# Performance work log

Hardware: AMD Instinct MI355X
Metric: run time of the kernel (lower is better)

Reference implementation:

```python
import jax, jax.numpy as jnp
import numpy as np

UNITS = 32      # 12 inter + 19 command + 1 motor
SENSORY = 32    # dense_2 output dim
MOTOR = 1
ODE_UNFOLDS = 6
EPS = 1e-8


def _build_wiring():
    # kerasncp NCP wiring: motor ids [0,1), command [1,20), inter [20,32)
    rng = np.random.RandomState(42)
    inter = np.arange(20, 32)
    command = np.arange(1, 20)
    motor = np.arange(0, 1)
    adj = np.zeros((UNITS, UNITS), np.float32)
    sens = np.zeros((SENSORY, UNITS), np.float32)
    for s in range(SENSORY):                      # sensory_fanout=6 onto inter neurons
        for d in rng.choice(inter, 6, replace=False):
            sens[s, d] = rng.choice([-1.0, 1.0])
    for i in inter:                               # inter_fanout=4 onto command neurons
        for d in rng.choice(command, 4, replace=False):
            adj[i, d] = rng.choice([-1.0, 1.0])
    for _ in range(6):                            # 6 recurrent command synapses
        adj[rng.choice(command), rng.choice(command)] = rng.choice([-1.0, 1.0])
    for m in motor:                               # motor_fanin=4 from command neurons
        for srcn in rng.choice(command, 4, replace=False):
            adj[srcn, m] = rng.choice([-1.0, 1.0])
    return adj, sens


def setup_inputs() -> dict:
    key = jax.random.key(0)
    ks = jax.random.split(key, 12)
    B, T = 256, 1024
    adj, sens = _build_wiring()
    u = lambda k, sh, lo, hi: jax.random.uniform(k, sh, jnp.float32, lo, hi)
    return {
        "x": jax.random.normal(ks[0], (B, T, 2), jnp.float32),
        "d1_w": jax.random.normal(ks[1], (2, 128), jnp.float32) * (1.0 / np.sqrt(2.0)),
        "d1_b": jnp.zeros((128,), jnp.float32),
        "d2_w": jax.random.normal(ks[2], (128, SENSORY), jnp.float32) * (1.0 / np.sqrt(128.0)),
        "d2_b": jnp.zeros((SENSORY,), jnp.float32),
        "input_w": jnp.ones((SENSORY,), jnp.float32),
        "input_b": jnp.zeros((SENSORY,), jnp.float32),
        "output_w": jnp.ones((MOTOR,), jnp.float32),
        "output_b": jnp.zeros((MOTOR,), jnp.float32),
        "gleak": u(ks[3], (UNITS,), 0.001, 1.0),
        "vleak": u(ks[4], (UNITS,), -0.2, 0.2),
        "cm": u(ks[5], (UNITS,), 0.4, 0.6),
        "w_syn": u(ks[6], (UNITS, UNITS), 0.001, 1.0),
        "mu": u(ks[7], (UNITS, UNITS), 0.3, 0.8),
        "sigma": u(ks[8], (UNITS, UNITS), 3.0, 8.0),
        "erev": jnp.asarray(adj),
        "sensory_w": u(ks[9], (SENSORY, UNITS), 0.001, 1.0),
        "sensory_mu": u(ks[10], (SENSORY, UNITS), 0.3, 0.8),
        "sensory_sigma": u(ks[11], (SENSORY, UNITS), 3.0, 8.0),
        "sensory_erev": jnp.asarray(sens),
        "sparsity_mask": jnp.asarray(np.abs(adj), jnp.int32),
        "sensory_mask": jnp.asarray(np.abs(sens), jnp.int32),
    }


def reference(x, d1_w, d1_b, d2_w, d2_b, input_w, input_b, output_w, output_b,
              gleak, vleak, cm, w_syn, mu, sigma, erev,
              sensory_w, sensory_mu, sensory_sigma, sensory_erev,
              sparsity_mask, sensory_mask):
    # Dense stack (per timestep)
    h = jax.nn.relu(x @ d1_w + d1_b)          # [B,T,128]
    h = h @ d2_w + d2_b                        # [B,T,32] sensory inputs
    spm = sparsity_mask.astype(h.dtype)
    ssm = sensory_mask.astype(h.dtype)

    def gate(v, m, s):                         # v [B,pre] -> [B,pre,post]
        return jax.nn.sigmoid(s * (v[..., None] - m))

    cm_t = cm * ODE_UNFOLDS                    # cm / (elapsed_time / ode_unfolds), elapsed_time=1

    def step(v, xt):
        inp = xt * input_w + input_b           # LTC input mapping (affine)
        sa = sensory_w * gate(inp, sensory_mu, sensory_sigma) * ssm   # [B,32,32]
        wnum_s = jnp.sum(sa * sensory_erev, axis=1)                   # [B,32]
        wden_s = jnp.sum(sa, axis=1)

        def unfold(vp, _):
            wa = w_syn * gate(vp, mu, sigma) * spm                    # [B,32,32]
            wnum = jnp.sum(wa * erev, axis=1) + wnum_s
            wden = jnp.sum(wa, axis=1) + wden_s
            vp = (cm_t * vp + gleak * vleak + wnum) / (cm_t + gleak + wden + EPS)
            return vp, None

        v, _ = jax.lax.scan(unfold, v, None, length=ODE_UNFOLDS)
        return v, None

    v0 = jnp.zeros((h.shape[0], UNITS), h.dtype)
    vT, _ = jax.lax.scan(step, v0, jnp.swapaxes(h, 0, 1))  # scan over T
    # output mapping: motor neurons are the first MOTOR states
    return vT[:, :MOTOR] * output_w + output_b             # [B,1]
```

## Files before the change

kernel.cpp:

```cpp
#include <hip/hip_runtime.h>
#include <math.h>

#define NB 256
#define NT 1024
#define NUNF 6
#define TBS 128
#define CHK 8
#define NTJMAX 12
#define L2E 1.44269504088896340736f
#define PI_F 3.14159265358979324f

typedef const float* fp;

extern "C" __device__ float __ocml_exp2_f32(float);
__device__ __forceinline__ float frcp(float x) { return __builtin_amdgcn_rcpf(x); }
__device__ __forceinline__ float ex2(float x) { return __ocml_exp2_f32(x); }
__device__ __forceinline__ float sgm(float a, float b, float v) { return frcp(1.f + ex2(fmaf(a, v, b))); }

struct Tables {
    int ngroups, npos, nchunks, ntraj;
    int grp_start[21];
    int ord[20];
    int pos[20];
    int aff[20];
    int need_traj[20];
    int traj_slot[20];
    int ch_ps[20], ch_pe[20], ch_gs[20], ch_ge[20];
    int ncp[20], nip[20], ngp[20];
    float cmt[20], cn0[20], cd0[20];
    float icmt[12];
    int   cp_pre[20][8];
    float cp_a[20][8], cp_b[20][8], cp_w[20][8], cp_e[20][8];
    int   ip_i[20][12];
    float ip_a[20][12], ip_b[20][12], ip_w[20][12], ip_e[20][12];
    int   gp_pre[20][6];
    float gp_a[20][6], gp_b[20][6], gp_w[20][6], gp_e[20][6];
};

struct DenseTab {
    int cnt[12];
    float in0[12], id0[12];
    int   pre[12][32];
    float a[12][32], b[12][32], w[12][32], e[12][32];
    int homog, maxcnt;
};

#define WS_DTAB   16384
#define WS_BND    24576
#define WS_BMASK  25600
#define WS_MG     32768
#define WS_VST    98304
#define WS_SENSI  131072

__global__ void build_tables(fp wsyn, fp mu, fp sigma, fp erev, const int* spm,
                             fp sw, fp smu, fp ssg, fp serev, const int* smask,
                             fp cm, fp gleak, fp vleak, fp d1b, Tables* T, DenseTab* D) {
    __shared__ int   spmL[1024], smkL[1024];
    __shared__ float wL[1024], muL[1024], sgL[1024], evL[1024];
    __shared__ float swL[1024], smuL[1024], ssgL[1024], sevL[1024];
    __shared__ float cmL[32], glL[32], vlL[32];
    __shared__ int premaskL[20], ancL[20], rootL[20], depUL[20], keyL[20], posL[20], ordL[20];
    __shared__ int ngpL[20], ntjL[20], slotU[20];
    __shared__ int neededS;
    __shared__ float habs[64];
    __shared__ int cntS[12];
    int tid = threadIdx.x;
    for (int k = tid; k < 1024; k += 64) {
        spmL[k] = spm[k]; wL[k] = wsyn[k]; muL[k] = mu[k]; sgL[k] = sigma[k]; evL[k] = erev[k];
        smkL[k] = smask[k]; swL[k] = sw[k]; smuL[k] = smu[k]; ssgL[k] = ssg[k]; sevL[k] = serev[k];
    }
    if (tid < 32) { cmL[tid] = cm[tid]; glL[tid] = gleak[tid]; vlL[tid] = vleak[tid]; }
    habs[tid] = fmaxf(fabsf(d1b[tid]), fabsf(d1b[tid + 64]));
    __syncthreads();
    if (tid < 20) {
        int pm = 0;
        for (int i = 0; i < 20; ++i) if (spmL[i * 32 + tid]) pm |= 1 << i;
        premaskL[tid] = pm;
        ancL[tid] = pm;
    }
    __syncthreads();
    for (int it = 0; it < 20; ++it) {
        int a = 0;
        if (tid < 20) {
            a = ancL[tid];
            int pm = premaskL[tid];
            for (int i = 0; i < 20; ++i) if ((pm >> i) & 1) a |= ancL[i];
        }
        __syncthreads();
        if (tid < 20) ancL[tid] = a;
        __syncthreads();
    }
    if (tid == 0) neededS = ancL[0] | 1;
    __syncthreads();
    int needed = neededS;
    if (tid < 20) {
        int r = tid;
        if ((needed >> tid) & 1) {
            int aj = ancL[tid];
            for (int i = 0; i < 20; ++i)
                if (i < r && ((needed >> i) & 1) && ((aj >> i) & 1) && ((ancL[i] >> tid) & 1)) r = i;
        }
        rootL[tid] = r;
        depUL[tid] = 0;
    }
    __syncthreads();
    for (int it = 0; it < 21; ++it) {
        int d = 0;
        if (tid < 20 && ((needed >> tid) & 1)) {
            int pm = premaskL[tid], myr = rootL[tid];
            for (int i = 0; i < 20; ++i)
                if (((pm >> i) & 1) && rootL[i] != myr) d = max(d, depUL[i] + 1);
        }
        __syncthreads();
        if (tid < 20 && d > depUL[tid]) depUL[tid] = d;
        __syncthreads();
    }
    if (tid < 20) {
        int key = 0x7FFFFFFF;
        if ((needed >> tid) & 1) {
            int myr = rootL[tid], dg = 0;
            for (int i = 0; i < 20; ++i)
                if (((needed >> i) & 1) && rootL[i] == myr) dg = max(dg, depUL[i]);
            key = dg * 32 + myr;
        }
        keyL[tid] = key;
    }
    __syncthreads();
    if (tid < 20) {
        int mykey = keyL[tid];
        int p = 0;
        for (int k = 0; k < 20; ++k)
            if (keyL[k] < mykey || (keyL[k] == mykey && k < tid)) ++p;
        posL[tid] = p;
        if (p < 20) ordL[p] = tid;
    }
    __syncthreads();
    if (tid < 20) {
        int nt = 0;
        if ((needed >> tid) & 1)
            for (int j = 0; j < 20; ++j)
                if (j != tid && ((needed >> j) & 1) && spmL[tid * 32 + j]) { nt = 1; break; }
        ntjL[tid] = nt;
    }
    __syncthreads();
    if (tid == 0) {
        int s = 0;
        for (int p = 0; p < 20; ++p) { int u = ordL[p]; slotU[u] = s; s += ntjL[u]; }
        T->ntraj = s;
    }
    __syncthreads();
    if (tid < 20) {
        int j = tid, cc = 0, ci = 0, cg = 0;
        T->cmt[j] = cmL[j] * (float)NUNF;
        T->cn0[j] = glL[j] * vlL[j];
        T->cd0[j] = cmL[j] * (float)NUNF + glL[j] + 1e-8f;
        if ((needed >> j) & 1) {
            int myr = rootL[j];
            int mystart = posL[myr];
            for (int i = 0; i < 32; ++i) {
                int p = i * 32 + j;
                if (!spmL[p]) continue;
                float sg = sgL[p];
                float a = -sg * L2E, b = sg * muL[p] * L2E;
                float w = wL[p], e = w * evL[p];
                if (i >= 20) {
                    T->ip_i[j][ci] = i - 20;
                    T->ip_a[j][ci] = a; T->ip_b[j][ci] = b; T->ip_w[j][ci] = w; T->ip_e[j][ci] = e;
                    ++ci;
                } else if (rootL[i] == myr) {
                    T->gp_pre[j][cg] = posL[i] - mystart;
                    T->gp_a[j][cg] = a; T->gp_b[j][cg] = b; T->gp_w[j][cg] = w; T->gp_e[j][cg] = e;
                    ++cg;
                } else {
                    T->cp_pre[j][cc] = slotU[i];
                    T->cp_a[j][cc] = a; T->cp_b[j][cc] = b; T->cp_w[j][cc] = w; T->cp_e[j][cc] = e;
                    ++cc;
                }
            }
        }
        T->ncp[j] = cc; T->nip[j] = ci; T->ngp[j] = cg;
        ngpL[j] = cg;
    }
    if (tid < 12) {
        T->icmt[tid] = cmL[20 + tid] * (float)NUNF;
        int unit = 20 + tid, cnt = 0;
        for (int s = 0; s < 32; ++s) {
            int p = s * 32 + unit;
            if (!smkL[p]) continue;
            float sg = ssgL[p];
            D->pre[tid][cnt] = s;
            D->a[tid][cnt] = -sg * L2E;
            D->b[tid][cnt] = sg * smuL[p] * L2E;
            D->w[tid][cnt] = swL[p];
            D->e[tid][cnt] = swL[p] * sevL[p];
            ++cnt;
        }
        for (int c = cnt; c < 32; ++c) {
            D->pre[tid][c] = 0; D->a[tid][c] = 0.f; D->b[tid][c] = 0.f;
            D->w[tid][c] = 0.f; D->e[tid][c] = 0.f;
        }
        D->cnt[tid] = cnt;
        cntS[tid] = cnt;
        D->in0[tid] = glL[unit] * vlL[unit];
        D->id0[tid] = cmL[unit] * (float)NUNF + glL[unit] + 1e-8f;
    }
    __syncthreads();
    if (tid == 0) {
        int npos = __popc(needed & 0xFFFFF);
        T->npos = npos;
        int ng = 0, prevkey = -1;
        for (int p = 0; p < npos; ++p) {
            int u = ordL[p];
            if (keyL[u] != prevkey) { T->grp_start[ng] = p; ++ng; prevkey = keyL[u]; }
        }
        T->ngroups = ng;
        for (int g = ng; g <= 20; ++g) T->grp_start[g] = npos;
        for (int p = 0; p < 20; ++p) T->ord[p] = (p < npos) ? ordL[p] : 0;
        for (int j = 0; j < 20; ++j) T->pos[j] = posL[j];
        for (int g = 0; g < ng; ++g) {
            int gs = T->grp_start[g], ge = T->grp_start[g + 1], gsz = ge - gs;
            for (int p = gs; p < ge; ++p)
                T->aff[p] = (gsz == 1 && ngpL[ordL[p]] == 0) ? 1 : 0;
        }
        for (int p = npos; p < 20; ++p) T->aff[p] = 0;
        for (int p = 0; p < 20; ++p) {
            int u = ordL[p];
            T->need_traj[p] = ntjL[u];
            T->traj_slot[p] = slotU[u];
        }
        int nchunks = 0, g = 0;
        while (g < ng) {
            int lvl = keyL[ordL[T->grp_start[g]]] / 32;
            int ge = g;
            while (ge < ng && keyL[ordL[T->grp_start[ge]]] / 32 == lvl) ++ge;
            int cs = g;
            while (cs < ge) {
                int ce = cs, acc = 0;
                while (ce < ge) {
                    int gsz = T->grp_start[ce + 1] - T->grp_start[ce];
                    if (acc + gsz > CHK && ce > cs) break;
                    acc += gsz; ++ce;
                    if (acc >= CHK) break;
                }
                T->ch_gs[nchunks] = cs; T->ch_ge[nchunks] = ce;
                T->ch_ps[nchunks] = T->grp_start[cs]; T->ch_pe[nchunks] = T->grp_start[ce];
                ++nchunks;
                cs = ce;
            }
            g = ge;
        }
        T->nchunks = nchunks;
        float hm = 0.f;
        for (int k = 0; k < 64; ++k) hm = fmaxf(hm, habs[k]);
        D->homog = (hm == 0.f) ? 1 : 0;
        int mc = 0;
        for (int k = 0; k < 12; ++k) mc = max(mc, cntS[k]);
        D->maxcnt = mc;
    }
}

__global__ void sector_prep(fp d1w, float* bnd, int* bmask) {
    __shared__ float ang[256];
    __shared__ float uS[128], vS[128];
    int tid = threadIdx.x;
    if (tid < 128) { uS[tid] = d1w[tid]; vS[tid] = d1w[128 + tid]; }
    __syncthreads();
    {
        int k = tid & 127;
        float al = atan2f(vS[k], uS[k]);
        float bb = (tid < 128) ? al + 1.57079632679489662f : al - 1.57079632679489662f;
        if (bb > PI_F) bb -= 2.f * PI_F;
        if (bb <= -PI_F) bb += 2.f * PI_F;
        ang[tid] = bb;
    }
    __syncthreads();
    for (int k = 2; k <= 256; k <<= 1) {
        for (int j = k >> 1; j > 0; j >>= 1) {
            int ixj = tid ^ j;
            if (ixj > tid) {
                float a0 = ang[tid], a1 = ang[ixj];
                bool up = ((tid & k) == 0);
                if ((a0 > a1) == up) { ang[tid] = a1; ang[ixj] = a0; }
            }
            __syncthreads();
        }
    }
    bnd[tid] = ang[tid];
    float lo = ang[tid];
    float hi = (tid < 255) ? ang[tid + 1] : ang[0] + 2.f * PI_F;
    float tm = 0.5f * (lo + hi);
    float ct = cosf(tm), st = sinf(tm);
    for (int w = 0; w < 4; ++w) {
        int m = 0;
        for (int kk = 0; kk < 32; ++kk) {
            int k = w * 32 + kk;
            if (fmaf(uS[k], ct, vS[k] * st) > 0.f) m |= 1 << kk;
        }
        bmask[tid * 4 + w] = m;
    }
}

__global__ void sector_M(fp d1w, fp d2w, fp iw, const int* bmask, float2* Mg) {
    int s = blockIdx.x, j = threadIdx.x;
    if (j >= 32) return;
    float acc0 = 0.f, acc1 = 0.f;
#pragma unroll
    for (int w = 0; w < 4; ++w) {
        int mm = bmask[s * 4 + w];
        for (int kk = 0; kk < 32; ++kk) {
            if ((mm >> kk) & 1) {
                int k = w * 32 + kk;
                float w2 = d2w[k * 32 + j];
                acc0 = fmaf(d1w[k], w2, acc0);
                acc1 = fmaf(d1w[128 + k], w2, acc1);
            }
        }
    }
    float iwj = iw[j];
    Mg[s * 32 + j] = make_float2(acc0 * iwj, acc1 * iwj);
}

__global__ __launch_bounds__(256) void dense_homog(
    fp x, fp d2b, fp iw, fp ib,
    const DenseTab* __restrict__ Dg, const float2* __restrict__ Mg, const float* __restrict__ bndg,
    float2* sensI, int t0, int CT) {
    if (Dg->homog == 0) return;
    __shared__ float bndL[256];
    __shared__ float4 tabT[416];
    __shared__ int   preT[416];
    __shared__ float ibuf[4][2112];
    __shared__ float b2q[32], iwq[32], ibq[32];
    __shared__ float in0L[12], id0L[12];
    int tid = threadIdx.x;
    for (int idx = tid; idx < 384; idx += 256) {
        int d = idx >> 5, e = idx & 31;
        int sl = e * 13 + d;
        tabT[sl] = make_float4(Dg->a[d][e], Dg->b[d][e], Dg->w[d][e], Dg->e[d][e]);
        preT[sl] = Dg->pre[d][e];
    }
    if (tid < 12) { in0L[tid] = Dg->in0[tid]; id0L[tid] = Dg->id0[tid]; }
    if (tid < 32) { b2q[tid] = d2b[tid]; iwq[tid] = iw[tid]; ibq[tid] = ib[tid]; }
    if (tid < 256) bndL[tid] = bndg[tid];
    __syncthreads();
    int wid = tid >> 6, lane = tid & 63;
    const float2* x2 = (const float2*)x;
    int gw = blockIdx.x * 4 + wid;
    int nw = gridDim.x * 4;
    float* ibf = ibuf[wid];
    int jj = lane & 31, h = lane >> 5;
    float cj = fmaf(b2q[jj], iwq[jj], ibq[jj]);
    int cntmax = Dg->maxcnt;
    int pass_total = (NB * CT) >> 6;
    for (int pass = gw; pass < pass_total; pass += nw) {
        int cg0 = pass * 64;
        int cg = cg0 + lane;
        int lt = cg >> 8, bb_ = cg & 255;
        float2 xv = x2[bb_ * NT + (t0 + lt)];
        float th = atan2f(xv.y, xv.x);
        int sec;
        if (th < bndL[0]) sec = 255;
        else {
            int lo = 0, hi = 255;
#pragma unroll
            for (int it7 = 0; it7 < 8; ++it7) {
                int mid = (lo + hi + 1) >> 1;
                if (bndL[mid] <= th) lo = mid; else hi = mid - 1;
            }
            sec = lo;
        }
        float x0r = xv.x, x1r = xv.y;
#pragma unroll 4
        for (int r = 0; r < 32; ++r) {
            int item = 2 * r + h;
            int s_it = __shfl(sec, item);
            float xi0 = __shfl(x0r, item);
            float xi1 = __shfl(x1r, item);
            float2 m = Mg[s_it * 32 + jj];
            ibf[item * 33 + jj] = fmaf(xi0, m.x, fmaf(xi1, m.y, cj));
        }
        __builtin_amdgcn_wave_barrier();
#pragma unroll
        for (int rb = 0; rb < 12; ++rb) {
            int task = rb * 64 + lane;
            int item = task / 12;
            int dd = task - item * 12;
            float wn = in0L[dd], wd = id0L[dd];
            for (int e = 0; e < cntmax; ++e) {
                int sl = e * 13 + dd;
                float4 tb = tabT[sl];
                float pv = ibf[item * 33 + preT[sl]];
                float gq = frcp(1.f + ex2(fmaf(tb.x, pv, tb.y)));
                wn = fmaf(tb.w, gq, wn);
                wd = fmaf(tb.z, gq, wd);
            }
            int cg2 = cg0 + item;
            int lt2 = cg2 >> 8, b2_ = cg2 & 255;
            sensI[(size_t)(b2_ * CT + lt2) * 12 + dd] = make_float2(wn, wd);
        }
        __builtin_amdgcn_wave_barrier();
    }
}

__global__ __launch_bounds__(256) void dense_general(
    fp x, fp d1w, fp d1b, fp d2w, fp d2b, fp iw, fp ib,
    const DenseTab* __restrict__ Dg, float2* sensI, int t0, int CT) {
    if (Dg->homog != 0) return;
    __shared__ float W2s[4096];
    __shared__ float W1s[256], b1s[128];
    __shared__ float b2q[32], iwq[32], ibq[32];
    __shared__ float4 tabT[416];
    __shared__ int   preT[416];
    __shared__ int   cntL[12];
    __shared__ float in0L[12], id0L[12];
    __shared__ float hbuf[4][128][20];
    __shared__ float ibuf[4][16][33];
    int tid = threadIdx.x;
    for (int idx = tid; idx < 384; idx += 256) {
        int d = idx >> 5, e = idx & 31;
        int sl = e * 13 + d;
        tabT[sl] = make_float4(Dg->a[d][e], Dg->b[d][e], Dg->w[d][e], Dg->e[d][e]);
        preT[sl] = Dg->pre[d][e];
    }
    if (tid < 12) { cntL[tid] = Dg->cnt[tid]; in0L[tid] = Dg->in0[tid]; id0L[tid] = Dg->id0[tid]; }
    for (int p = tid; p < 4096; p += 256) W2s[p] = d2w[p];
    if (tid < 256) W1s[tid] = d1w[tid];
    if (tid < 128) b1s[tid] = d1b[tid];
    if (tid < 32) { b2q[tid] = d2b[tid]; iwq[tid] = iw[tid]; ibq[tid] = ib[tid]; }
    __syncthreads();
    int wid = tid >> 6, lane = tid & 63;
    float* hb = (float*)hbuf[wid];
    float* ibf = (float*)ibuf[wid];
    const float2* x2 = (const float2*)x;
    int gw = blockIdx.x * 4 + wid;
    int nw = gridDim.x * 4;
    int pass_total = (NB * CT) >> 4;
    int itd1 = lane >> 2, kq = lane & 3;
    int j = lane & 31, half = lane >> 5;
    for (int pass = gw; pass < pass_total; pass += nw) {
        int cg0 = pass * 16;
        {
            int cg = cg0 + itd1;
            int lt = cg >> 8, b = cg & 255;
            float2 xv = x2[b * NT + (t0 + lt)];
#pragma unroll 8
            for (int i = 0; i < 32; ++i) {
                int k = kq + 4 * i;
                float hk = fmaf(xv.y, W1s[128 + k], fmaf(xv.x, W1s[k], b1s[k]));
                hb[k * 20 + itd1] = hk > 0.f ? hk : 0.f;
            }
        }
        __builtin_amdgcn_wave_barrier();
        {
            float a0=0,a1=0,a2=0,a3=0,a4=0,a5=0,a6=0,a7=0;
#pragma unroll 4
            for (int k = 0; k < 128; ++k) {
                float w2 = W2s[k * 32 + j];
                float4 ha = *(const float4*)&hb[k * 20 + half * 8];
                float4 hbv = *(const float4*)&hb[k * 20 + half * 8 + 4];
                a0 = fmaf(ha.x, w2, a0); a1 = fmaf(ha.y, w2, a1);
                a2 = fmaf(ha.z, w2, a2); a3 = fmaf(ha.w, w2, a3);
                a4 = fmaf(hbv.x, w2, a4); a5 = fmaf(hbv.y, w2, a5);
                a6 = fmaf(hbv.z, w2, a6); a7 = fmaf(hbv.w, w2, a7);
            }
            float bb = b2q[j], iww = iwq[j], ibb = ibq[j];
            ibf[(half*8+0)*33+j] = fmaf(a0+bb, iww, ibb);
            ibf[(half*8+1)*33+j] = fmaf(a1+bb, iww, ibb);
            ibf[(half*8+2)*33+j] = fmaf(a2+bb, iww, ibb);
            ibf[(half*8+3)*33+j] = fmaf(a3+bb, iww, ibb);
            ibf[(half*8+4)*33+j] = fmaf(a4+bb, iww, ibb);
            ibf[(half*8+5)*33+j] = fmaf(a5+bb, iww, ibb);
            ibf[(half*8+6)*33+j] = fmaf(a6+bb, iww, ibb);
            ibf[(half*8+7)*33+j] = fmaf(a7+bb, iww, ibb);
        }
        __builtin_amdgcn_wave_barrier();
#pragma unroll
        for (int r = 0; r < 3; ++r) {
            int task = r * 64 + lane;
            int it = task / 12;
            int d = task - it * 12;
            int cnt = cntL[d];
            float wn = in0L[d], wd = id0L[d];
            for (int e = 0; e < cnt; ++e) {
                int sl = e * 13 + d;
                float4 tb = tabT[sl];
                float gq = frcp(1.f + ex2(fmaf(tb.x, ibf[it * 33 + preT[sl]], tb.y)));
                wn = fmaf(tb.w, gq, wn);
                wd = fmaf(tb.z, gq, wd);
            }
            int cg = cg0 + it;
            int lt = cg >> 8, b = cg & 255;
            sensI[(size_t)(b * CT + lt) * 12 + d] = make_float2(wn, wd);
        }
        __builtin_amdgcn_wave_barrier();
    }
}

__global__ __launch_bounds__(512) void solve(const float2* __restrict__ sensI,
                                             const Tables* __restrict__ Tg,
                                             fp ow, fp ob, float* vstate,
                                             int t0, int CT, float* out) {
    __shared__ Tables TL;
    __shared__ float2 iAB[TBS * 12];
    __shared__ float viter[TBS * 13];
    __shared__ float vtraj[NTJMAX * TBS * 7];
    __shared__ float2 pnpd[CHK * TBS * 7];
    __shared__ float2 comp[CHK * TBS];
    __shared__ float vstart[CHK * TBS];
    __shared__ float gstate[20], istate[12];
    int tid = threadIdx.x;
    int b = blockIdx.x;
    {
        const int nw = (int)(sizeof(Tables) / 4);
        const int* src = (const int*)Tg;
        int* dst = (int*)&TL;
        for (int k = tid; k < nw; k += 512) dst[k] = src[k];
    }
    __syncthreads();
    if (tid < 20 && tid < TL.npos)
        gstate[tid] = (t0 == 0) ? 0.f : vstate[b * 32 + TL.ord[tid]];
    if (tid < 12)
        istate[tid] = (t0 == 0) ? 0.f : vstate[b * 32 + 20 + tid];
    __syncthreads();
    int ntiles = CT / TBS;
    bool lastChunk = (t0 + CT == NT);
    for (int tile = 0; tile < ntiles; ++tile) {
        int tbase = tile * TBS;
        for (int w = tid; w < TBS * 16; w += 512) {
            int tt = w >> 4, ii = w & 15;
            if (ii < 12) {
                float2 s = sensI[(size_t)(b * CT + tbase + tt) * 12 + ii];
                float r = frcp(s.y);
                iAB[tt * 12 + ii] = make_float2(TL.icmt[ii] * r, s.x * r);
            }
        }
        __syncthreads();
        if (tid < 12) {
            float v = istate[tid];
#pragma unroll 4
            for (int tt = 0; tt < TBS; ++tt) {
                float2 ab = iAB[tt * 12 + tid];
                float A = ab.x, B = ab.y;
                float A2 = A * A, A4 = A2 * A2;
                float A6 = A4 * A2;
                float B6 = B * (1.f + A) * (1.f + A2 + A4);
                viter[tt * 13 + tid] = v;
                v = fmaf(A6, v, B6);
            }
            istate[tid] = v;
        }
        __syncthreads();
        int nchunks = TL.nchunks;
        for (int c = 0; c < nchunks; ++c) {
            int ps = TL.ch_ps[c], pe = TL.ch_pe[c];
            int gs0 = TL.ch_gs[c], ge0 = TL.ch_ge[c];
            int npc = pe - ps;
            for (int w = tid; w < npc * TBS; w += 512) {
                int m = w >> 7, tt = w & (TBS - 1);
                int posi = ps + m;
                int unit = TL.ord[posi];
                float pn[6], pd[6];
#pragma unroll
                for (int u = 0; u < 6; ++u) { pn[u] = TL.cn0[unit]; pd[u] = TL.cd0[unit]; }
                int ncp = TL.ncp[unit];
                for (int e = 0; e < ncp; ++e) {
                    int sl = TL.cp_pre[unit][e];
                    float a = TL.cp_a[unit][e], bb = TL.cp_b[unit][e];
                    float w_ = TL.cp_w[unit][e], ev = TL.cp_e[unit][e];
#pragma unroll
                    for (int u = 0; u < 6; ++u) {
                        float gq = sgm(a, bb, vtraj[(sl * TBS + tt) * 7 + u]);
                        pn[u] = fmaf(ev, gq, pn[u]);
                        pd[u] = fmaf(w_, gq, pd[u]);
                    }
                }
                int nip = TL.nip[unit];
                for (int e = 0; e < nip; ++e) {
                    int ii = TL.ip_i[unit][e];
                    float2 ab = iAB[tt * 12 + ii];
                    float vi = viter[tt * 13 + ii];
                    float a = TL.ip_a[unit][e], bb = TL.ip_b[unit][e];
                    float w_ = TL.ip_w[unit][e], ev = TL.ip_e[unit][e];
#pragma unroll
                    for (int u = 0; u < 6; ++u) {
                        float gq = sgm(a, bb, vi);
                        pn[u] = fmaf(ev, gq, pn[u]);
                        pd[u] = fmaf(w_, gq, pd[u]);
                        vi = fmaf(ab.x, vi, ab.y);
                    }
                }
                if (TL.aff[posi]) {
                    float cmt = TL.cmt[unit];
                    float Ac = 1.f, Bc = 0.f;
#pragma unroll
                    for (int u = 0; u < 6; ++u) {
                        float r = frcp(pd[u]);
                        float Au = cmt * r, Bu = pn[u] * r;
                        pnpd[(m * TBS + tt) * 7 + u] = make_float2(Au, Bu);
                        Bc = fmaf(Au, Bc, Bu);
                        Ac *= Au;
                    }
                    comp[m * TBS + tt] = make_float2(Ac, Bc);
                } else {
#pragma unroll
                    for (int u = 0; u < 6; ++u)
                        pnpd[(m * TBS + tt) * 7 + u] = make_float2(pn[u], pd[u]);
                }
            }
            __syncthreads();
            if (tid < ge0 - gs0) {
                int g = gs0 + tid;
                int gs = TL.grp_start[g], ge = TL.grp_start[g + 1], gsz = ge - gs;
                int m0 = gs - ps;
                if (gsz == 1) {
                    int unit = TL.ord[gs];
                    float v = gstate[gs];
                    if (TL.aff[gs]) {
#pragma unroll 4
                        for (int tt = 0; tt < TBS; ++tt) {
                            vstart[m0 * TBS + tt] = v;
                            float2 cc = comp[m0 * TBS + tt];
                            v = fmaf(cc.x, v, cc.y);
                        }
                    } else {
                        float ga = TL.gp_a[unit][0], gb = TL.gp_b[unit][0];
                        float gw = TL.gp_w[unit][0], gev = TL.gp_e[unit][0];
                        float cmt = TL.cmt[unit];
                        int ntj = TL.need_traj[gs];
                        int sl = TL.traj_slot[gs];
                        for (int tt = 0; tt < TBS; ++tt) {
#pragma unroll
                            for (int u = 0; u < 6; ++u) {
                                if (ntj) vtraj[(sl * TBS + tt) * 7 + u] = v;
                                float2 pp2 = pnpd[(m0 * TBS + tt) * 7 + u];
                                float E = ex2(fmaf(ga, v, gb));
                                float P = fmaf(cmt, v, pp2.x);
                                float N = fmaf(P, E, P + gev);
                                float Dd = fmaf(pp2.y, E, pp2.y + gw);
                                v = N * frcp(Dd);
                            }
                        }
                    }
                    gstate[gs] = v;
                } else {
                    float sv[CHK], nv[CHK];
#pragma unroll
                    for (int mm = 0; mm < CHK; ++mm) if (mm < gsz) sv[mm] = gstate[gs + mm];
                    for (int tt = 0; tt < TBS; ++tt) {
#pragma unroll
                        for (int u = 0; u < 6; ++u) {
#pragma unroll
                            for (int mm = 0; mm < CHK; ++mm)
                                if (mm < gsz && TL.need_traj[gs + mm])
                                    vtraj[(TL.traj_slot[gs + mm] * TBS + tt) * 7 + u] = sv[mm];
#pragma unroll
                            for (int mm = 0; mm < CHK; ++mm) {
                                if (mm < gsz) {
                                    int unit = TL.ord[gs + mm];
                                    float2 pp2 = pnpd[((m0 + mm) * TBS + tt) * 7 + u];
                                    float wn = pp2.x, wd = pp2.y;
                                    int ngpu = TL.ngp[unit];
#pragma unroll
                                    for (int e = 0; e < 6; ++e) {
                                        if (e < ngpu) {
                                            float vp = sv[TL.gp_pre[unit][e]];
                                            float gq = sgm(TL.gp_a[unit][e], TL.gp_b[unit][e], vp);
                                            wn = fmaf(TL.gp_e[unit][e], gq, wn);
                                            wd = fmaf(TL.gp_w[unit][e], gq, wd);
                                        }
                                    }
                                    nv[mm] = fmaf(TL.cmt[unit], sv[mm], wn) * frcp(wd);
                                }
                            }
#pragma unroll
                            for (int mm = 0; mm < CHK; ++mm) if (mm < gsz) sv[mm] = nv[mm];
                        }
                    }
#pragma unroll
                    for (int mm = 0; mm < CHK; ++mm) if (mm < gsz) gstate[gs + mm] = sv[mm];
                }
            }
            __syncthreads();
            for (int w = tid; w < npc * TBS; w += 512) {
                int m = w >> 7, tt = w & (TBS - 1);
                int posi = ps + m;
                if (TL.aff[posi] && TL.need_traj[posi]) {
                    int sl = TL.traj_slot[posi];
                    float v = vstart[m * TBS + tt];
#pragma unroll
                    for (int u = 0; u < 6; ++u) {
                        vtraj[(sl * TBS + tt) * 7 + u] = v;
                        float2 ab = pnpd[(m * TBS + tt) * 7 + u];
                        v = fmaf(ab.x, v, ab.y);
                    }
                }
            }
            __syncthreads();
        }
    }
    if (tid < 20 && tid < TL.npos) vstate[b * 32 + TL.ord[tid]] = gstate[tid];
    if (tid < 12) vstate[b * 32 + 20 + tid] = istate[tid];
    if (lastChunk) {
        __syncthreads();
        if (tid == 0) out[b] = fmaf(gstate[TL.pos[0]], ow[0], ob[0]);
    }
}

extern "C" void kernel_launch(void* const* d_in, const int* in_sizes, int n_in,
                              void* d_out, int out_size, void* d_ws, size_t ws_size,
                              hipStream_t stream) {
    fp x     = (fp)d_in[0];
    fp d1w   = (fp)d_in[1];
    fp d1b   = (fp)d_in[2];
    fp d2w   = (fp)d_in[3];
    fp d2b   = (fp)d_in[4];
    fp iw    = (fp)d_in[5];
    fp ib    = (fp)d_in[6];
    fp ow    = (fp)d_in[7];
    fp ob    = (fp)d_in[8];
    fp gleak = (fp)d_in[9];
    fp vleak = (fp)d_in[10];
    fp cm    = (fp)d_in[11];
    fp wsyn  = (fp)d_in[12];
    fp mu    = (fp)d_in[13];
    fp sigma = (fp)d_in[14];
    fp erev  = (fp)d_in[15];
    fp sw    = (fp)d_in[16];
    fp smu   = (fp)d_in[17];
    fp ssg   = (fp)d_in[18];
    fp serev = (fp)d_in[19];
    const int* spm   = (const int*)d_in[20];
    const int* smask = (const int*)d_in[21];

    char* wsb = (char*)d_ws;
    Tables*   T = (Tables*)wsb;
    DenseTab* D = (DenseTab*)(wsb + WS_DTAB);
    float*   bnd = (float*)(wsb + WS_BND);
    int*   bmask = (int*)(wsb + WS_BMASK);
    float2*   Mg = (float2*)(wsb + WS_MG);
    float* vstate = (float*)(wsb + WS_VST);
    float2* sensI = (float2*)(wsb + WS_SENSI);

    size_t per_t = (size_t)NB * 12 * sizeof(float2);
    int CT = TBS;
    if (ws_size > WS_SENSI) {
        size_t m = (ws_size - WS_SENSI) / per_t;
        int ct = TBS;
        while (ct < NT && (size_t)(ct * 2) <= m) ct *= 2;
        CT = ct;
    }

    build_tables<<<1, 64, 0, stream>>>(wsyn, mu, sigma, erev, spm,
                                       sw, smu, ssg, serev, smask,
                                       cm, gleak, vleak, d1b, T, D);
    sector_prep<<<1, 256, 0, stream>>>(d1w, bnd, bmask);
    sector_M<<<256, 64, 0, stream>>>(d1w, d2w, iw, bmask, Mg);

    int nch = NT / CT;
    for (int c = 0; c < nch; ++c) {
        int t0 = c * CT;
        dense_homog<<<768, 256, 0, stream>>>(x, d2b, iw, ib, D, Mg, bnd, sensI, t0, CT);
        dense_general<<<512, 256, 0, stream>>>(x, d1w, d1b, d2w, d2b, iw, ib, D, sensI, t0, CT);
        solve<<<NB, 512, 0, stream>>>(sensI, T, ow, ob, vstate, t0, CT, (float*)d_out);
    }
}
```

Before: 276.0 us.

## Fuse homogeneous sensory dense stage into the solve kernel per tile

Removes the separate dense_homog kernel and computes the sensory synapse sums inside solve for each 128-step tile, writing iAB directly from shared memory instead of round-tripping through the global sensI buffer. This drops one launch per chunk and the global write/read of the sensory intermediates. In exchange, the per-batch solve block now does the atan2, sector search and gating work itself, serially before each tile's recurrence, which adds shared-memory pressure and lengthens the solve kernel's critical path.

```diff
diff --git a/kernel.cpp b/kernel.cpp
--- a/kernel.cpp
+++ b/kernel.cpp
@@ -320,87 +320,6 @@
     Mg[s * 32 + j] = make_float2(acc0 * iwj, acc1 * iwj);
 }
 
-__global__ __launch_bounds__(256) void dense_homog(
-    fp x, fp d2b, fp iw, fp ib,
-    const DenseTab* __restrict__ Dg, const float2* __restrict__ Mg, const float* __restrict__ bndg,
-    float2* sensI, int t0, int CT) {
-    if (Dg->homog == 0) return;
-    __shared__ float bndL[256];
-    __shared__ float4 tabT[416];
-    __shared__ int   preT[416];
-    __shared__ float ibuf[4][2112];
-    __shared__ float b2q[32], iwq[32], ibq[32];
-    __shared__ float in0L[12], id0L[12];
-    int tid = threadIdx.x;
-    for (int idx = tid; idx < 384; idx += 256) {
-        int d = idx >> 5, e = idx & 31;
-        int sl = e * 13 + d;
-        tabT[sl] = make_float4(Dg->a[d][e], Dg->b[d][e], Dg->w[d][e], Dg->e[d][e]);
-        preT[sl] = Dg->pre[d][e];
-    }
-    if (tid < 12) { in0L[tid] = Dg->in0[tid]; id0L[tid] = Dg->id0[tid]; }
-    if (tid < 32) { b2q[tid] = d2b[tid]; iwq[tid] = iw[tid]; ibq[tid] = ib[tid]; }
-    if (tid < 256) bndL[tid] = bndg[tid];
-    __syncthreads();
-    int wid = tid >> 6, lane = tid & 63;
-    const float2* x2 = (const float2*)x;
-    int gw = blockIdx.x * 4 + wid;
-    int nw = gridDim.x * 4;
-    float* ibf = ibuf[wid];
-    int jj = lane & 31, h = lane >> 5;
-    float cj = fmaf(b2q[jj], iwq[jj], ibq[jj]);
-    int cntmax = Dg->maxcnt;
-    int pass_total = (NB * CT) >> 6;
-    for (int pass = gw; pass < pass_total; pass += nw) {
-        int cg0 = pass * 64;
-        int cg = cg0 + lane;
-        int lt = cg >> 8, bb_ = cg & 255;
-        float2 xv = x2[bb_ * NT + (t0 + lt)];
-        float th = atan2f(xv.y, xv.x);
-        int sec;
-        if (th < bndL[0]) sec = 255;
-        else {
-            int lo = 0, hi = 255;
-#pragma unroll
-            for (int it7 = 0; it7 < 8; ++it7) {
-                int mid = (lo + hi + 1) >> 1;
-                if (bndL[mid] <= th) lo = mid; else hi = mid - 1;
-            }
-            sec = lo;
-        }
-        float x0r = xv.x, x1r = xv.y;
-#pragma unroll 4
-        for (int r = 0; r < 32; ++r) {
-            int item = 2 * r + h;
-            int s_it = __shfl(sec, item);
-            float xi0 = __shfl(x0r, item);
-            float xi1 = __shfl(x1r, item);
-            float2 m = Mg[s_it * 32 + jj];
-            ibf[item * 33 + jj] = fmaf(xi0, m.x, fmaf(xi1, m.y, cj));
-        }
-        __builtin_amdgcn_wave_barrier();
-#pragma unroll
-        for (int rb = 0; rb < 12; ++rb) {
-            int task = rb * 64 + lane;
-            int item = task / 12;
-            int dd = task - item * 12;
-            float wn = in0L[dd], wd = id0L[dd];
-            for (int e = 0; e < cntmax; ++e) {
-                int sl = e * 13 + dd;
-                float4 tb = tabT[sl];
-                float pv = ibf[item * 33 + preT[sl]];
-                float gq = frcp(1.f + ex2(fmaf(tb.x, pv, tb.y)));
-                wn = fmaf(tb.w, gq, wn);
-                wd = fmaf(tb.z, gq, wd);
-            }
-            int cg2 = cg0 + item;
-            int lt2 = cg2 >> 8, b2_ = cg2 & 255;
-            sensI[(size_t)(b2_ * CT + lt2) * 12 + dd] = make_float2(wn, wd);
-        }
-        __builtin_amdgcn_wave_barrier();
-    }
-}
-
 __global__ __launch_bounds__(256) void dense_general(
     fp x, fp d1w, fp d1b, fp d2w, fp d2b, fp iw, fp ib,
     const DenseTab* __restrict__ Dg, float2* sensI, int t0, int CT) {
@@ -495,10 +414,12 @@
     }
 }
 
-__global__ __launch_bounds__(512) void solve(const float2* __restrict__ sensI,
-                                             const Tables* __restrict__ Tg,
-                                             fp ow, fp ob, float* vstate,
-                                             int t0, int CT, float* out) {
+__global__ __launch_bounds__(512) void solve(
+    fp x, const float2* __restrict__ sensI,
+    const Tables* __restrict__ Tg, const DenseTab* __restrict__ Dg,
+    const float2* __restrict__ Mg, const float* __restrict__ bndg,
+    fp d2b, fp iw, fp ib,
+    fp ow, fp ob, float* vstate, int t0, int CT, float* out) {
     __shared__ Tables TL;
     __shared__ float2 iAB[TBS * 12];
     __shared__ float viter[TBS * 13];
@@ -507,6 +428,11 @@
     __shared__ float2 comp[CHK * TBS];
     __shared__ float vstart[CHK * TBS];
     __shared__ float gstate[20], istate[12];
+    __shared__ float bndL[256];
+    __shared__ float4 tabT[416];
+    __shared__ int   preT[416];
+    __shared__ float b2qL[32], iwqL[32], ibqL[32];
+    __shared__ float in0L[12], id0L[12];
     int tid = threadIdx.x;
     int b = blockIdx.x;
     {
@@ -515,6 +441,19 @@
         int* dst = (int*)&TL;
         for (int k = tid; k < nw; k += 512) dst[k] = src[k];
     }
+    int homog = Dg->homog;
+    int cntmax = Dg->maxcnt;
+    if (homog) {
+        for (int idx = tid; idx < 384; idx += 512) {
+            int d = idx >> 5, e = idx & 31;
+            int sl = e * 13 + d;
+            tabT[sl] = make_float4(Dg->a[d][e], Dg->b[d][e], Dg->w[d][e], Dg->e[d][e]);
+            preT[sl] = Dg->pre[d][e];
+        }
+        if (tid < 256) bndL[tid] = bndg[tid];
+        if (tid < 32) { b2qL[tid] = d2b[tid]; iwqL[tid] = iw[tid]; ibqL[tid] = ib[tid]; }
+        if (tid < 12) { in0L[tid] = Dg->in0[tid]; id0L[tid] = Dg->id0[tid]; }
+    }
     __syncthreads();
     if (tid < 20 && tid < TL.npos)
         gstate[tid] = (t0 == 0) ? 0.f : vstate[b * 32 + TL.ord[tid]];
@@ -523,14 +462,59 @@
     __syncthreads();
     int ntiles = CT / TBS;
     bool lastChunk = (t0 + CT == NT);
+    const float2* x2 = (const float2*)x;
     for (int tile = 0; tile < ntiles; ++tile) {
         int tbase = tile * TBS;
-        for (int w = tid; w < TBS * 16; w += 512) {
-            int tt = w >> 4, ii = w & 15;
-            if (ii < 12) {
-                float2 s = sensI[(size_t)(b * CT + tbase + tt) * 12 + ii];
-                float r = frcp(s.y);
-                iAB[tt * 12 + ii] = make_float2(TL.icmt[ii] * r, s.x * r);
+        if (homog) {
+            float* ibufL = (float*)pnpd;
+            {
+                int item = tid >> 2, q = tid & 3;
+                float2 xv = x2[(size_t)b * NT + (t0 + tbase + item)];
+                float th = atan2f(xv.y, xv.x);
+                int sec;
+                if (th < bndL[0]) sec = 255;
+                else {
+                    int lo = 0, hi = 255;
+#pragma unroll
+                    for (int it7 = 0; it7 < 8; ++it7) {
+                        int mid = (lo + hi + 1) >> 1;
+                        if (bndL[mid] <= th) lo = mid; else hi = mid - 1;
+                    }
+                    sec = lo;
+                }
+#pragma unroll
+                for (int c = 0; c < 8; ++c) {
+                    int j = q * 8 + c;
+                    float2 m = Mg[sec * 32 + j];
+                    float cj = fmaf(b2qL[j], iwqL[j], ibqL[j]);
+                    ibufL[item * 33 + j] = fmaf(xv.x, m.x, fmaf(xv.y, m.y, cj));
+                }
+            }
+            __syncthreads();
+#pragma unroll
+            for (int rb = 0; rb < 3; ++rb) {
+                int task = rb * 512 + tid;
+                int item = task / 12;
+                int dd = task - item * 12;
+                float wn = in0L[dd], wd = id0L[dd];
+                for (int e = 0; e < cntmax; ++e) {
+                    int sl = e * 13 + dd;
+                    float4 tb = tabT[sl];
+                    float gq = frcp(1.f + ex2(fmaf(tb.x, ibufL[item * 33 + preT[sl]], tb.y)));
+                    wn = fmaf(tb.w, gq, wn);
+                    wd = fmaf(tb.z, gq, wd);
+                }
+                float r = frcp(wd);
+                iAB[item * 12 + dd] = make_float2(TL.icmt[dd] * r, wn * r);
+            }
+        } else {
+            for (int w = tid; w < TBS * 16; w += 512) {
+                int tt = w >> 4, ii = w & 15;
+                if (ii < 12) {
+                    float2 s = sensI[(size_t)(b * CT + tbase + tt) * 12 + ii];
+                    float r = frcp(s.y);
+                    iAB[tt * 12 + ii] = make_float2(TL.icmt[ii] * r, s.x * r);
+                }
             }
         }
         __syncthreads();
@@ -758,8 +742,8 @@
     int nch = NT / CT;
     for (int c = 0; c < nch; ++c) {
         int t0 = c * CT;
-        dense_homog<<<768, 256, 0, stream>>>(x, d2b, iw, ib, D, Mg, bnd, sensI, t0, CT);
         dense_general<<<512, 256, 0, stream>>>(x, d1w, d1b, d2w, d2b, iw, ib, D, sensI, t0, CT);
-        solve<<<NB, 512, 0, stream>>>(sensI, T, ow, ob, vstate, t0, CT, (float*)d_out);
+        solve<<<NB, 512, 0, stream>>>(x, sensI, T, D, Mg, bnd, d2b, iw, ib,
+                                      ow, ob, vstate, t0, CT, (float*)d_out);
     }
 }
```

Measured after the change: 249.2 us. -9.7%, faster.
